# Optimization experiments

Hardware: AMD Instinct MI355X
Metric: run time of the kernel (lower is better)

## Reference

```python
import jax, jax.numpy as jnp
import numpy as np

V, L, E, H = 32000, 32, 512, 512   # vocab, nb_labels, emb_dim, hidden per direction (hidden_dim//2)
B, T = 128, 512
BOS_TAG, EOS_TAG = 1, 2


def setup_inputs() -> dict:
    key = jax.random.key(0)
    ks = jax.random.split(key, 10)
    def s(k, shape, scale=0.05):
        return jax.random.normal(k, shape, dtype=jnp.float32) * scale
    return {
        "x": jax.random.randint(ks[0], (B, T), 0, V),
        "mask": jnp.ones((B, T), jnp.int32),
        "emb": s(ks[1], (V, E), 0.1),
        "W_ih_f": s(ks[2], (4 * H, E)), "W_hh_f": s(ks[3], (4 * H, H)), "b_f": jnp.zeros((4 * H,), jnp.float32),
        "W_ih_b": s(ks[4], (4 * H, E)), "W_hh_b": s(ks[5], (4 * H, H)), "b_b": jnp.zeros((4 * H,), jnp.float32),
        "W_out": s(ks[6], (L, 2 * H)), "b_out": jnp.zeros((L,), jnp.float32),
        "transitions": s(ks[7], (L, L), 0.1),
    }


def _lstm_dir(x_emb, W_ih, W_hh, b, reverse):
    # x_emb: [B, T, E] -> hidden states [B, T, H]
    Bn = x_emb.shape[0]
    Hn = W_hh.shape[1]
    def cell(carry, x_t):
        h, c = carry
        g = x_t @ W_ih.T + h @ W_hh.T + b          # [B, 4H]
        i, f, gg, o = jnp.split(g, 4, axis=-1)
        c = jax.nn.sigmoid(f) * c + jax.nn.sigmoid(i) * jnp.tanh(gg)
        h = jax.nn.sigmoid(o) * jnp.tanh(c)
        return (h, c), h
    init = (jnp.zeros((Bn, Hn), x_emb.dtype), jnp.zeros((Bn, Hn), x_emb.dtype))
    _, hs = jax.lax.scan(cell, init, x_emb.transpose(1, 0, 2), reverse=reverse)
    return hs.transpose(1, 0, 2)


def _emissions(x, emb, W_ih_f, W_hh_f, b_f, W_ih_b, W_hh_b, b_b, W_out, b_out):
    xe = emb[x]                                    # [B, T, E]
    hf = _lstm_dir(xe, W_ih_f, W_hh_f, b_f, False)
    hb = _lstm_dir(xe, W_ih_b, W_hh_b, b_b, True)
    h = jnp.concatenate([hf, hb], axis=-1)         # [B, T, 2H]
    return h @ W_out.T + b_out                     # [B, T, L]


def _viterbi_decode(em, trans, mask):
    # em: [B, T, L]; trans[prev, next]; returns (score [B], path [B, T])
    m = mask.astype(em.dtype)
    alphas = trans[BOS_TAG][None, :] + em[:, 0]    # [B, L]
    def step(alphas, inp):
        e_t, m_t = inp                             # [B, L], [B]
        scores = alphas[:, :, None] + trans[None] + e_t[:, None, :]  # [B, Lprev, Lnext]
        new = scores.max(axis=1)
        bp = scores.argmax(axis=1).astype(jnp.int32)
        alphas = m_t[:, None] * new + (1.0 - m_t[:, None]) * alphas
        return alphas, (bp, m_t)
    alphas, (bps, ms) = jax.lax.scan(
        step, alphas, (em[:, 1:].transpose(1, 0, 2), m[:, 1:].T))
    final = alphas + trans[:, EOS_TAG][None, :]
    score = final.max(axis=-1)                     # [B]
    last_tag = final.argmax(axis=-1).astype(jnp.int32)
    def back(tag, inp):
        bp_t, m_t = inp
        prev = jnp.take_along_axis(bp_t, tag[:, None], axis=1)[:, 0]
        tag = jnp.where(m_t > 0, prev, tag)
        return tag, tag
    _, traced = jax.lax.scan(back, last_tag, (bps, ms), reverse=True)  # [T-1, B]
    path = jnp.concatenate([traced.transpose(1, 0), last_tag[:, None]], axis=1)
    return score, path


def reference(x, mask, emb, W_ih_f, W_hh_f, b_f, W_ih_b, W_hh_b, b_b, W_out, b_out, transitions):
    em = _emissions(x, emb, W_ih_f, W_hh_f, b_f, W_ih_b, W_hh_b, b_b, W_out, b_out)
    return _viterbi_decode(em, transitions, mask)
```

## Files before the change

### kernel.cpp

```cpp
#include <hip/hip_runtime.h>
#include <math.h>

namespace {
constexpr int BATCH = 128;
constexpr int SEQ   = 512;
constexpr int NL    = 32;
constexpr int BOSTAG = 1;
constexpr int EOSTAG = 2;
}

#define AL(p)    __hip_atomic_load((p),       __ATOMIC_RELAXED, __HIP_MEMORY_SCOPE_AGENT)
#define AS(p, v) __hip_atomic_store((p), (v), __ATOMIC_RELAXED, __HIP_MEMORY_SCOPE_AGENT)
#define AADD(p)  __hip_atomic_fetch_add((p), 1u, __ATOMIC_RELAXED, __HIP_MEMORY_SCOPE_AGENT)

__device__ unsigned g_sub[4][8][32];
__device__ unsigned g_root[4][32];

__global__ void reset_cnt_kernel() {
  const int i = threadIdx.x;
  ((unsigned*)g_sub)[i] = 0u;
  if (i < 4 * 32) ((unsigned*)g_root)[i] = 0u;
}

__device__ __forceinline__ void gbar(int g, int sub, unsigned epoch) {
  __syncthreads();
  if (threadIdx.x == 0) {
    const unsigned old = AADD(&g_sub[g][sub][0]);
    if (old == 8u * epoch - 1u)
      AADD(&g_root[g][0]);
    while (AL(&g_root[g][0]) < 8u * epoch)
      __builtin_amdgcn_s_sleep(2);
  }
  __builtin_amdgcn_fence(__ATOMIC_ACQUIRE, "agent");
  __syncthreads();
}

__global__ __launch_bounds__(512, 1)
void bilstm_coop(const int* __restrict__ x,
                 const float* __restrict__ emb,
                 const float* __restrict__ Wih_f, const float* __restrict__ Whh_f, const float* __restrict__ bf,
                 const float* __restrict__ Wih_b, const float* __restrict__ Whh_b, const float* __restrict__ bbias,
                 const float* __restrict__ Wout, const float* __restrict__ bout,
                 float* __restrict__ hbuf, float* __restrict__ em)
{
  __shared__ float4 WT4[8192];
  __shared__ float  em_red[512];
  float* WTf = (float*)WT4;

  const int tid = threadIdx.x, bi = blockIdx.x;
  const int rX = bi & 7, qX = bi >> 3;
  const int grp = rX >> 1;
  const int dir = grp >> 1, bh = grp & 1;
  const int ug  = (qX << 1) | (rX & 1);
  const int u0  = ug * 8, b_base = bh * 64;
  const int bb  = b_base + ug;
  const int sub = ug >> 3;

  const float* Wih = dir ? Wih_b : Wih_f;
  const float* Whh = dir ? Whh_b : Whh_f;
  const float* bv  = dir ? bbias : bf;

  for (int idx = tid; idx < 32768; idx += 512) {
    const int k = idx >> 5, r = idx & 31;
    const int gate = r & 3, uu = r >> 2;
    const int grow = gate * 512 + u0 + uu;
    const float v = (k < 512) ? Wih[(size_t)grow * 512 + k]
                              : Whh[(size_t)grow * 512 + (k - 512)];
    WTf[k * 32 + ((uu ^ ((k >> 2) & 7)) << 2) + gate] = v;
  }

  const int ks   = tid & 7;
  const int ug2  = (tid >> 3) & 3;
  const int bq   = ((tid >> 5) & 1) + 2 * (tid >> 6);
  const int bB   = b_base + 4 * bq;
  const int wb0 = 32 * ks + ((2 * ug2 + 0) ^ ks);
  const int wb1 = 32 * ks + ((2 * ug2 + 1) ^ ks);
  const int u_own = u0 + 2 * ug2 + (ks & 1);
  const int b_own = bB + (ks >> 1);
  const int l_ = tid >> 4, kc = tid & 15;

  float bias_g[4];
  #pragma unroll
  for (int g = 0; g < 4; ++g) bias_g[g] = bv[g * 512 + u_own];
  float cstate = 0.f;

  AS(&hbuf[131072 + dir * 65536 + (size_t)bb * 512 + tid], 0.f);
  unsigned epoch = 1;
  gbar(grp, sub, epoch); ++epoch;

  for (int s = 0; s < SEQ; ++s) {
    const int t = dir ? (SEQ - 1 - s) : s;

    const float* e0 = emb + (size_t)x[(bB + 0) * SEQ + t] * 512 + 4 * ks;
    const float* e1 = emb + (size_t)x[(bB + 1) * SEQ + t] * 512 + 4 * ks;
    const float* e2 = emb + (size_t)x[(bB + 2) * SEQ + t] * 512 + 4 * ks;
    const float* e3 = emb + (size_t)x[(bB + 3) * SEQ + t] * 512 + 4 * ks;
    float4 cur[4], nxt[4];
    cur[0] = *(const float4*)e0; cur[1] = *(const float4*)e1;
    cur[2] = *(const float4*)e2; cur[3] = *(const float4*)e3;

    gbar(grp, sub, epoch); ++epoch;

    const float* hprev = hbuf + (size_t)((s + 1) & 1) * 131072 + dir * 65536;
    float*       hout  = hbuf + (size_t)((s    ) & 1) * 131072 + dir * 65536;

    if (s > 0) {
      const float* hb2 = hprev + (size_t)bb * 512 + kc * 32;
      float4 hq[8];
      #pragma unroll
      for (int q = 0; q < 8; ++q) hq[q] = *(const float4*)(hb2 + q * 4);
      const float* wr_ = Wout + (size_t)l_ * 1024 + dir * 512 + kc * 32;
      float emP = 0.f;
      #pragma unroll
      for (int q = 0; q < 8; ++q) {
        const float4 wv = *(const float4*)&wr_[q * 4];
        emP = fmaf(hq[q].x, wv.x, emP);
        emP = fmaf(hq[q].y, wv.y, emP);
        emP = fmaf(hq[q].z, wv.z, emP);
        emP = fmaf(hq[q].w, wv.w, emP);
      }
      em_red[kc * 32 + l_] = emP;
    }
    __syncthreads();
    if (s > 0 && tid < 32) {
      float p = 0.f;
      #pragma unroll
      for (int ksi = 0; ksi < 16; ++ksi) p += em_red[ksi * 32 + tid];
      const int te = dir ? (SEQ - s) : (s - 1);
      if (!dir) p += bout[tid];
      atomicAdd(em + ((size_t)bb * SEQ + te) * NL + tid, p);
    }

    const float* h0 = hprev + (size_t)(bB + 0) * 512 + 4 * ks;
    const float* h1 = hprev + (size_t)(bB + 1) * 512 + 4 * ks;
    const float* h2 = hprev + (size_t)(bB + 2) * 512 + 4 * ks;
    const float* h3 = hprev + (size_t)(bB + 3) * 512 + 4 * ks;

    float acc0[4][4], acc1[4][4];
    #pragma unroll
    for (int r = 0; r < 4; ++r)
      #pragma unroll
      for (int g = 0; g < 4; ++g) { acc0[r][g] = 0.f; acc1[r][g] = 0.f; }

    #pragma unroll 2
    for (int i = 0; i < 16; ++i) {
      if (i < 15) {
        nxt[0] = *(const float4*)(e0 + (i + 1) * 32);
        nxt[1] = *(const float4*)(e1 + (i + 1) * 32);
        nxt[2] = *(const float4*)(e2 + (i + 1) * 32);
        nxt[3] = *(const float4*)(e3 + (i + 1) * 32);
      } else {
        nxt[0] = *(const float4*)h0; nxt[1] = *(const float4*)h1;
        nxt[2] = *(const float4*)h2; nxt[3] = *(const float4*)h3;
      }
      #pragma unroll
      for (int j = 0; j < 4; ++j) {
        const float4 w0 = WT4[wb0 + 256 * i + 8 * j];
        const float4 w1 = WT4[wb1 + 256 * i + 8 * j];
        #pragma unroll
        for (int r = 0; r < 4; ++r) {
          const float a = (j == 0) ? cur[r].x : (j == 1) ? cur[r].y : (j == 2) ? cur[r].z : cur[r].w;
          acc0[r][0] = fmaf(w0.x, a, acc0[r][0]);
          acc0[r][1] = fmaf(w0.y, a, acc0[r][1]);
          acc0[r][2] = fmaf(w0.z, a, acc0[r][2]);
          acc0[r][3] = fmaf(w0.w, a, acc0[r][3]);
          acc1[r][0] = fmaf(w1.x, a, acc1[r][0]);
          acc1[r][1] = fmaf(w1.y, a, acc1[r][1]);
          acc1[r][2] = fmaf(w1.z, a, acc1[r][2]);
          acc1[r][3] = fmaf(w1.w, a, acc1[r][3]);
        }
      }
      #pragma unroll
      for (int r = 0; r < 4; ++r) cur[r] = nxt[r];
    }
    #pragma unroll 2
    for (int i = 0; i < 16; ++i) {
      if (i < 15) {
        nxt[0] = *(const float4*)(h0 + (i + 1) * 32);
        nxt[1] = *(const float4*)(h1 + (i + 1) * 32);
        nxt[2] = *(const float4*)(h2 + (i + 1) * 32);
        nxt[3] = *(const float4*)(h3 + (i + 1) * 32);
      }
      #pragma unroll
      for (int j = 0; j < 4; ++j) {
        const float4 w0 = WT4[4096 + wb0 + 256 * i + 8 * j];
        const float4 w1 = WT4[4096 + wb1 + 256 * i + 8 * j];
        #pragma unroll
        for (int r = 0; r < 4; ++r) {
          const float a = (j == 0) ? cur[r].x : (j == 1) ? cur[r].y : (j == 2) ? cur[r].z : cur[r].w;
          acc0[r][0] = fmaf(w0.x, a, acc0[r][0]);
          acc0[r][1] = fmaf(w0.y, a, acc0[r][1]);
          acc0[r][2] = fmaf(w0.z, a, acc0[r][2]);
          acc0[r][3] = fmaf(w0.w, a, acc0[r][3]);
          acc1[r][0] = fmaf(w1.x, a, acc1[r][0]);
          acc1[r][1] = fmaf(w1.y, a, acc1[r][1]);
          acc1[r][2] = fmaf(w1.z, a, acc1[r][2]);
          acc1[r][3] = fmaf(w1.w, a, acc1[r][3]);
        }
      }
      #pragma unroll
      for (int r = 0; r < 4; ++r) cur[r] = nxt[r];
    }

    #pragma unroll
    for (int m = 1; m < 8; m <<= 1)
      #pragma unroll
      for (int r = 0; r < 4; ++r)
        #pragma unroll
        for (int g = 0; g < 4; ++g) {
          acc0[r][g] += __shfl_xor(acc0[r][g], m, 64);
          acc1[r][g] += __shfl_xor(acc1[r][g], m, 64);
        }

    {
      float g4[4];
      #pragma unroll
      for (int g = 0; g < 4; ++g) {
        float v = acc0[0][g];
        v = (ks == 1) ? acc1[0][g] : v;
        v = (ks == 2) ? acc0[1][g] : v;
        v = (ks == 3) ? acc1[1][g] : v;
        v = (ks == 4) ? acc0[2][g] : v;
        v = (ks == 5) ? acc1[2][g] : v;
        v = (ks == 6) ? acc0[3][g] : v;
        v = (ks == 7) ? acc1[3][g] : v;
        g4[g] = v;
      }
      const float gi = g4[0] + bias_g[0];
      const float gf = g4[1] + bias_g[1];
      const float gg = g4[2] + bias_g[2];
      const float go = g4[3] + bias_g[3];
      const float si = 1.f / (1.f + expf(-gi));
      const float sf = 1.f / (1.f + expf(-gf));
      const float so = 1.f / (1.f + expf(-go));
      cstate = sf * cstate + si * tanhf(gg);
      AS(&hout[(size_t)b_own * 512 + u_own], so * tanhf(cstate));
    }
  }
  gbar(grp, sub, epoch); ++epoch;

  {
    const float* hb2 = hbuf + 131072 + dir * 65536 + (size_t)bb * 512 + kc * 32;
    const float* wr_ = Wout + (size_t)l_ * 1024 + dir * 512 + kc * 32;
    float emP = 0.f;
    #pragma unroll
    for (int q = 0; q < 8; ++q) {
      const float4 hv = *(const float4*)(hb2 + q * 4);
      const float4 wv = *(const float4*)&wr_[q * 4];
      emP = fmaf(hv.x, wv.x, emP);
      emP = fmaf(hv.y, wv.y, emP);
      emP = fmaf(hv.z, wv.z, emP);
      emP = fmaf(hv.w, wv.w, emP);
    }
    em_red[kc * 32 + l_] = emP;
    __syncthreads();
    if (tid < 32) {
      float p = 0.f;
      #pragma unroll
      for (int ksi = 0; ksi < 16; ++ksi) p += em_red[ksi * 32 + tid];
      const int te = dir ? 0 : (SEQ - 1);
      if (!dir) p += bout[tid];
      atomicAdd(em + ((size_t)bb * SEQ + te) * NL + tid, p);
    }
  }
}

__global__ __launch_bounds__(64)
void viterbi_kernel(const float* __restrict__ em, const int* __restrict__ mask,
                    const float* __restrict__ trans, float* __restrict__ out)
{
  __shared__ float tr[32][33];
  __shared__ float alpha[32];
  __shared__ float fin[32];
  __shared__ unsigned char bp[SEQ][32];
  __shared__ float path[SEQ];

  const int b = blockIdx.x, tid = threadIdx.x;
  for (int i = tid; i < 1024; i += 64) tr[i >> 5][i & 31] = trans[i];
  __syncthreads();

  const float* emB = em + (size_t)b * SEQ * NL;
  if (tid < 32) alpha[tid] = tr[BOSTAG][tid] + emB[tid];
  __syncthreads();

  for (int t = 1; t < SEQ; ++t) {
    float best = -INFINITY, e = 0.f;
    int arg = 0;
    if (tid < 32) {
      e = emB[t * NL + tid];
      #pragma unroll 4
      for (int p = 0; p < 32; ++p) {
        const float sc = (alpha[p] + tr[p][tid]) + e;
        if (sc > best) { best = sc; arg = p; }
      }
    }
    __syncthreads();
    if (tid < 32) {
      const float m = (float)mask[b * SEQ + t];
      alpha[tid] = m * best + (1.f - m) * alpha[tid];
      bp[t][tid] = (unsigned char)arg;
    }
    __syncthreads();
  }

  if (tid < 32) fin[tid] = alpha[tid] + tr[tid][EOSTAG];
  __syncthreads();

  if (tid == 0) {
    float best = fin[0]; int tag = 0;
    for (int n = 1; n < 32; ++n) if (fin[n] > best) { best = fin[n]; tag = n; }
    out[b] = best;
    path[SEQ - 1] = (float)tag;
    for (int k = SEQ - 2; k >= 0; --k) {
      const int prev = bp[k + 1][tag];
      if (mask[b * SEQ + k + 1] > 0) tag = prev;
      path[k] = (float)tag;
    }
  }
  __syncthreads();
  for (int idx = tid; idx < SEQ; idx += 64)
    out[BATCH + (size_t)b * SEQ + idx] = path[idx];
}

extern "C" void kernel_launch(void* const* d_in, const int* in_sizes, int n_in,
                              void* d_out, int out_size, void* d_ws, size_t ws_size,
                              hipStream_t stream) {
  (void)in_sizes; (void)n_in; (void)out_size; (void)ws_size;
  const int*   x     = (const int*)d_in[0];
  const int*   mask  = (const int*)d_in[1];
  const float* emb   = (const float*)d_in[2];
  const float* Wih_f = (const float*)d_in[3];
  const float* Whh_f = (const float*)d_in[4];
  const float* bf    = (const float*)d_in[5];
  const float* Wih_b = (const float*)d_in[6];
  const float* Whh_b = (const float*)d_in[7];
  const float* bb    = (const float*)d_in[8];
  const float* Wout  = (const float*)d_in[9];
  const float* bout  = (const float*)d_in[10];
  const float* trans = (const float*)d_in[11];
  float* out  = (float*)d_out;
  float* hbuf = (float*)d_ws;
  float* em   = hbuf + 262144;

  reset_cnt_kernel<<<dim3(1), dim3(1024), 0, stream>>>();
  hipMemsetAsync(em, 0, (size_t)2097152 * sizeof(float), stream);

  void* args[] = { (void*)&x, (void*)&emb,
                   (void*)&Wih_f, (void*)&Whh_f, (void*)&bf,
                   (void*)&Wih_b, (void*)&Whh_b, (void*)&bb,
                   (void*)&Wout, (void*)&bout,
                   (void*)&hbuf, (void*)&em };
  hipLaunchCooperativeKernel((void*)bilstm_coop, dim3(256), dim3(512), args, 0, stream);
  viterbi_kernel<<<dim3(128), dim3(64), 0, stream>>>(em, mask, trans, out);
}
```

Measured before the change: 20.66 ms.

## Split LSTM work into 1024-thread blocks handling both directions with 4 units each

Each block now runs 1024 threads, the two halves serving the forward and backward direction, and owns 4 hidden units instead of 8. That halves per-thread FMA work and weight tile per direction. The grid barrier groups drop from four to two, with 16 sub-counters per group. The aim is more threads per CU to hide latency and less serial arithmetic per step, at the cost of barriers spanning twice as many blocks and a reworked weight layout in LDS.

```diff
diff --git a/kernel.cpp b/kernel.cpp
--- a/kernel.cpp
+++ b/kernel.cpp
@@ -13,13 +13,13 @@
 #define AS(p, v) __hip_atomic_store((p), (v), __ATOMIC_RELAXED, __HIP_MEMORY_SCOPE_AGENT)
 #define AADD(p)  __hip_atomic_fetch_add((p), 1u, __ATOMIC_RELAXED, __HIP_MEMORY_SCOPE_AGENT)
 
-__device__ unsigned g_sub[4][8][32];
-__device__ unsigned g_root[4][32];
+__device__ unsigned g_sub[2][16][32];
+__device__ unsigned g_root[2][32];
 
 __global__ void reset_cnt_kernel() {
   const int i = threadIdx.x;
   ((unsigned*)g_sub)[i] = 0u;
-  if (i < 4 * 32) ((unsigned*)g_root)[i] = 0u;
+  if (i < 64) ((unsigned*)g_root)[i] = 0u;
 }
 
 __device__ __forceinline__ void gbar(int g, int sub, unsigned epoch) {
@@ -28,14 +28,14 @@
     const unsigned old = AADD(&g_sub[g][sub][0]);
     if (old == 8u * epoch - 1u)
       AADD(&g_root[g][0]);
-    while (AL(&g_root[g][0]) < 8u * epoch)
+    while (AL(&g_root[g][0]) < 16u * epoch)
       __builtin_amdgcn_s_sleep(2);
   }
   __builtin_amdgcn_fence(__ATOMIC_ACQUIRE, "agent");
   __syncthreads();
 }
 
-__global__ __launch_bounds__(512, 1)
+__global__ __launch_bounds__(1024, 4)
 void bilstm_coop(const int* __restrict__ x,
                  const float* __restrict__ emb,
                  const float* __restrict__ Wih_f, const float* __restrict__ Whh_f, const float* __restrict__ bf,
@@ -43,50 +43,62 @@
                  const float* __restrict__ Wout, const float* __restrict__ bout,
                  float* __restrict__ hbuf, float* __restrict__ em)
 {
-  __shared__ float4 WT4[8192];
-  __shared__ float  em_red[512];
-  float* WTf = (float*)WT4;
+  __shared__ float4 WT4[2][4096];
+  __shared__ float  em_red[2][512];
 
   const int tid = threadIdx.x, bi = blockIdx.x;
-  const int rX = bi & 7, qX = bi >> 3;
-  const int grp = rX >> 1;
-  const int dir = grp >> 1, bh = grp & 1;
-  const int ug  = (qX << 1) | (rX & 1);
-  const int u0  = ug * 8, b_base = bh * 64;
-  const int bb  = b_base + ug;
-  const int sub = ug >> 3;
+  const int dir = tid >> 9;
+  const int tl  = tid & 511;
+  const int bh  = bi & 1;
+  const int ublock = bi >> 1;
+  const int u0  = ublock * 4, b_base = bh * 64;
+  const int p   = ublock & 1;
+  const int bb  = b_base + (ublock >> 1);
+  const int sub = ublock >> 3;
 
   const float* Wih = dir ? Wih_b : Wih_f;
   const float* Whh = dir ? Whh_b : Whh_f;
   const float* bv  = dir ? bbias : bf;
 
-  for (int idx = tid; idx < 32768; idx += 512) {
-    const int k = idx >> 5, r = idx & 31;
-    const int gate = r & 3, uu = r >> 2;
-    const int grow = gate * 512 + u0 + uu;
-    const float v = (k < 512) ? Wih[(size_t)grow * 512 + k]
-                              : Whh[(size_t)grow * 512 + (k - 512)];
-    WTf[k * 32 + ((uu ^ ((k >> 2) & 7)) << 2) + gate] = v;
-  }
-
-  const int ks   = tid & 7;
-  const int ug2  = (tid >> 3) & 3;
-  const int bq   = ((tid >> 5) & 1) + 2 * (tid >> 6);
+  {
+    float4* WTd = WT4[dir];
+    for (int n = tl; n < 4096; n += 512) {
+      const int k = n >> 2, uu = n & 3;
+      const int idx = ((k >> 3) << 5) + (((k >> 2) & 1) << 2) + ((k & 3) << 3) + uu;
+      float4 v;
+      if (k < 512) {
+        v.x = Wih[(size_t)(0 * 512 + u0 + uu) * 512 + k];
+        v.y = Wih[(size_t)(1 * 512 + u0 + uu) * 512 + k];
+        v.z = Wih[(size_t)(2 * 512 + u0 + uu) * 512 + k];
+        v.w = Wih[(size_t)(3 * 512 + u0 + uu) * 512 + k];
+      } else {
+        const int kk = k - 512;
+        v.x = Whh[(size_t)(0 * 512 + u0 + uu) * 512 + kk];
+        v.y = Whh[(size_t)(1 * 512 + u0 + uu) * 512 + kk];
+        v.z = Whh[(size_t)(2 * 512 + u0 + uu) * 512 + kk];
+        v.w = Whh[(size_t)(3 * 512 + u0 + uu) * 512 + kk];
+      }
+      WTd[idx] = v;
+    }
+  }
+  const float4* WTd = WT4[dir];
+
+  const int ks   = tl & 7;
+  const int ug2  = (tl >> 3) & 3;
+  const int bq   = tl >> 5;
   const int bB   = b_base + 4 * bq;
-  const int wb0 = 32 * ks + ((2 * ug2 + 0) ^ ks);
-  const int wb1 = 32 * ks + ((2 * ug2 + 1) ^ ks);
-  const int u_own = u0 + 2 * ug2 + (ks & 1);
-  const int b_own = bB + (ks >> 1);
-  const int l_ = tid >> 4, kc = tid & 15;
+  const int wb   = ((ks >> 1) << 5) + ((ks & 1) << 2) + ug2;
+  const int l_ = tl >> 4, kc = tl & 15;
 
   float bias_g[4];
   #pragma unroll
-  for (int g = 0; g < 4; ++g) bias_g[g] = bv[g * 512 + u_own];
+  for (int g = 0; g < 4; ++g) bias_g[g] = bv[g * 512 + u0 + ug2];
   float cstate = 0.f;
 
-  AS(&hbuf[131072 + dir * 65536 + (size_t)bb * 512 + tid], 0.f);
+  if (tl < 256)
+    AS(&hbuf[131072 + dir * 65536 + (size_t)bb * 512 + p * 256 + tl], 0.f);
   unsigned epoch = 1;
-  gbar(grp, sub, epoch); ++epoch;
+  gbar(bh, sub, epoch); ++epoch;
 
   for (int s = 0; s < SEQ; ++s) {
     const int t = dir ? (SEQ - 1 - s) : s;
@@ -99,36 +111,34 @@
     cur[0] = *(const float4*)e0; cur[1] = *(const float4*)e1;
     cur[2] = *(const float4*)e2; cur[3] = *(const float4*)e3;
 
-    gbar(grp, sub, epoch); ++epoch;
+    gbar(bh, sub, epoch); ++epoch;
 
     const float* hprev = hbuf + (size_t)((s + 1) & 1) * 131072 + dir * 65536;
     float*       hout  = hbuf + (size_t)((s    ) & 1) * 131072 + dir * 65536;
 
     if (s > 0) {
-      const float* hb2 = hprev + (size_t)bb * 512 + kc * 32;
-      float4 hq[8];
-      #pragma unroll
-      for (int q = 0; q < 8; ++q) hq[q] = *(const float4*)(hb2 + q * 4);
-      const float* wr_ = Wout + (size_t)l_ * 1024 + dir * 512 + kc * 32;
+      const float* hb2 = hprev + (size_t)bb * 512 + p * 256 + kc * 16;
+      const float* wr_ = Wout + (size_t)l_ * 1024 + dir * 512 + p * 256 + kc * 16;
       float emP = 0.f;
       #pragma unroll
-      for (int q = 0; q < 8; ++q) {
-        const float4 wv = *(const float4*)&wr_[q * 4];
-        emP = fmaf(hq[q].x, wv.x, emP);
-        emP = fmaf(hq[q].y, wv.y, emP);
-        emP = fmaf(hq[q].z, wv.z, emP);
-        emP = fmaf(hq[q].w, wv.w, emP);
-      }
-      em_red[kc * 32 + l_] = emP;
+      for (int q = 0; q < 4; ++q) {
+        const float4 hv = *(const float4*)(hb2 + q * 4);
+        const float4 wv = *(const float4*)(wr_ + q * 4);
+        emP = fmaf(hv.x, wv.x, emP);
+        emP = fmaf(hv.y, wv.y, emP);
+        emP = fmaf(hv.z, wv.z, emP);
+        emP = fmaf(hv.w, wv.w, emP);
+      }
+      em_red[dir][kc * 32 + l_] = emP;
     }
     __syncthreads();
-    if (s > 0 && tid < 32) {
-      float p = 0.f;
-      #pragma unroll
-      for (int ksi = 0; ksi < 16; ++ksi) p += em_red[ksi * 32 + tid];
+    if (s > 0 && tl < 32) {
+      float pr = 0.f;
+      #pragma unroll
+      for (int ksi = 0; ksi < 16; ++ksi) pr += em_red[dir][ksi * 32 + tl];
       const int te = dir ? (SEQ - s) : (s - 1);
-      if (!dir) p += bout[tid];
-      atomicAdd(em + ((size_t)bb * SEQ + te) * NL + tid, p);
+      if (!dir && p == 0) pr += bout[tl];
+      atomicAdd(em + ((size_t)bb * SEQ + te) * NL + tl, pr);
     }
 
     const float* h0 = hprev + (size_t)(bB + 0) * 512 + 4 * ks;
@@ -136,11 +146,11 @@
     const float* h2 = hprev + (size_t)(bB + 2) * 512 + 4 * ks;
     const float* h3 = hprev + (size_t)(bB + 3) * 512 + 4 * ks;
 
-    float acc0[4][4], acc1[4][4];
+    float acc[4][4];
     #pragma unroll
     for (int r = 0; r < 4; ++r)
       #pragma unroll
-      for (int g = 0; g < 4; ++g) { acc0[r][g] = 0.f; acc1[r][g] = 0.f; }
+      for (int g = 0; g < 4; ++g) acc[r][g] = 0.f;
 
     #pragma unroll 2
     for (int i = 0; i < 16; ++i) {
@@ -155,19 +165,15 @@
       }
       #pragma unroll
       for (int j = 0; j < 4; ++j) {
-        const float4 w0 = WT4[wb0 + 256 * i + 8 * j];
-        const float4 w1 = WT4[wb1 + 256 * i + 8 * j];
+        const float4 w0 = WTd[wb + 128 * i + 8 * j];
         #pragma unroll
         for (int r = 0; r < 4; ++r) {
-          const float a = (j == 0) ? cur[r].x : (j == 1) ? cur[r].y : (j == 2) ? cur[r].z : cur[r].w;
-          acc0[r][0] = fmaf(w0.x, a, acc0[r][0]);
-          acc0[r][1] = fmaf(w0.y, a, acc0[r][1]);
-          acc0[r][2] = fmaf(w0.z, a, acc0[r][2]);
-          acc0[r][3] = fmaf(w0.w, a, acc0[r][3]);
-          acc1[r][0] = fmaf(w1.x, a, acc1[r][0]);
-          acc1[r][1] = fmaf(w1.y, a, acc1[r][1]);
-          acc1[r][2] = fmaf(w1.z, a, acc1[r][2]);
-          acc1[r][3] = fmaf(w1.w, a, acc1[r][3]);
+          const float a = (j == 0) ? cur[r].x : (j == 1) ? cur[r].y
+                        : (j == 2) ? cur[r].z : cur[r].w;
+          acc[r][0] = fmaf(w0.x, a, acc[r][0]);
+          acc[r][1] = fmaf(w0.y, a, acc[r][1]);
+          acc[r][2] = fmaf(w0.z, a, acc[r][2]);
+          acc[r][3] = fmaf(w0.w, a, acc[r][3]);
         }
       }
       #pragma unroll
@@ -183,19 +189,15 @@
       }
       #pragma unroll
       for (int j = 0; j < 4; ++j) {
-        const float4 w0 = WT4[4096 + wb0 + 256 * i + 8 * j];
-        const float4 w1 = WT4[4096 + wb1 + 256 * i + 8 * j];
+        const float4 w0 = WTd[2048 + wb + 128 * i + 8 * j];
         #pragma unroll
         for (int r = 0; r < 4; ++r) {
-          const float a = (j == 0) ? cur[r].x : (j == 1) ? cur[r].y : (j == 2) ? cur[r].z : cur[r].w;
-          acc0[r][0] = fmaf(w0.x, a, acc0[r][0]);
-          acc0[r][1] = fmaf(w0.y, a, acc0[r][1]);
-          acc0[r][2] = fmaf(w0.z, a, acc0[r][2]);
-          acc0[r][3] = fmaf(w0.w, a, acc0[r][3]);
-          acc1[r][0] = fmaf(w1.x, a, acc1[r][0]);
-          acc1[r][1] = fmaf(w1.y, a, acc1[r][1]);
-          acc1[r][2] = fmaf(w1.z, a, acc1[r][2]);
-          acc1[r][3] = fmaf(w1.w, a, acc1[r][3]);
+          const float a = (j == 0) ? cur[r].x : (j == 1) ? cur[r].y
+                        : (j == 2) ? cur[r].z : cur[r].w;
+          acc[r][0] = fmaf(w0.x, a, acc[r][0]);
+          acc[r][1] = fmaf(w0.y, a, acc[r][1]);
+          acc[r][2] = fmaf(w0.z, a, acc[r][2]);
+          acc[r][3] = fmaf(w0.w, a, acc[r][3]);
         }
       }
       #pragma unroll
@@ -207,23 +209,17 @@
       #pragma unroll
       for (int r = 0; r < 4; ++r)
         #pragma unroll
-        for (int g = 0; g < 4; ++g) {
-          acc0[r][g] += __shfl_xor(acc0[r][g], m, 64);
-          acc1[r][g] += __shfl_xor(acc1[r][g], m, 64);
-        }
+        for (int g = 0; g < 4; ++g)
+          acc[r][g] += __shfl_xor(acc[r][g], m, 64);
 
     {
       float g4[4];
       #pragma unroll
       for (int g = 0; g < 4; ++g) {
-        float v = acc0[0][g];
-        v = (ks == 1) ? acc1[0][g] : v;
-        v = (ks == 2) ? acc0[1][g] : v;
-        v = (ks == 3) ? acc1[1][g] : v;
-        v = (ks == 4) ? acc0[2][g] : v;
-        v = (ks == 5) ? acc1[2][g] : v;
-        v = (ks == 6) ? acc0[3][g] : v;
-        v = (ks == 7) ? acc1[3][g] : v;
+        float v = acc[0][g];
+        v = (ks == 1) ? acc[1][g] : v;
+        v = (ks == 2) ? acc[2][g] : v;
+        v = (ks == 3) ? acc[3][g] : v;
         g4[g] = v;
       }
       const float gi = g4[0] + bias_g[0];
@@ -234,33 +230,34 @@
       const float sf = 1.f / (1.f + expf(-gf));
       const float so = 1.f / (1.f + expf(-go));
       cstate = sf * cstate + si * tanhf(gg);
-      AS(&hout[(size_t)b_own * 512 + u_own], so * tanhf(cstate));
-    }
-  }
-  gbar(grp, sub, epoch); ++epoch;
+      if (ks < 4)
+        AS(&hout[(size_t)(bB + ks) * 512 + u0 + ug2], so * tanhf(cstate));
+    }
+  }
+  gbar(bh, sub, epoch); ++epoch;
 
   {
-    const float* hb2 = hbuf + 131072 + dir * 65536 + (size_t)bb * 512 + kc * 32;
-    const float* wr_ = Wout + (size_t)l_ * 1024 + dir * 512 + kc * 32;
+    const float* hb2 = hbuf + 131072 + dir * 65536 + (size_t)bb * 512 + p * 256 + kc * 16;
+    const float* wr_ = Wout + (size_t)l_ * 1024 + dir * 512 + p * 256 + kc * 16;
     float emP = 0.f;
     #pragma unroll
-    for (int q = 0; q < 8; ++q) {
+    for (int q = 0; q < 4; ++q) {
       const float4 hv = *(const float4*)(hb2 + q * 4);
-      const float4 wv = *(const float4*)&wr_[q * 4];
+      const float4 wv = *(const float4*)(wr_ + q * 4);
       emP = fmaf(hv.x, wv.x, emP);
       emP = fmaf(hv.y, wv.y, emP);
       emP = fmaf(hv.z, wv.z, emP);
       emP = fmaf(hv.w, wv.w, emP);
     }
-    em_red[kc * 32 + l_] = emP;
+    em_red[dir][kc * 32 + l_] = emP;
     __syncthreads();
-    if (tid < 32) {
-      float p = 0.f;
-      #pragma unroll
-      for (int ksi = 0; ksi < 16; ++ksi) p += em_red[ksi * 32 + tid];
+    if (tl < 32) {
+      float pr = 0.f;
+      #pragma unroll
+      for (int ksi = 0; ksi < 16; ++ksi) pr += em_red[dir][ksi * 32 + tl];
       const int te = dir ? 0 : (SEQ - 1);
-      if (!dir) p += bout[tid];
-      atomicAdd(em + ((size_t)bb * SEQ + te) * NL + tid, p);
+      if (!dir && p == 0) pr += bout[tl];
+      atomicAdd(em + ((size_t)bb * SEQ + te) * NL + tl, pr);
     }
   }
 }
@@ -350,6 +347,6 @@
                    (void*)&Wih_b, (void*)&Whh_b, (void*)&bb,
                    (void*)&Wout, (void*)&bout,
                    (void*)&hbuf, (void*)&em };
-  hipLaunchCooperativeKernel((void*)bilstm_coop, dim3(256), dim3(512), args, 0, stream);
+  hipLaunchCooperativeKernel((void*)bilstm_coop, dim3(256), dim3(1024), args, 0, stream);
   viterbi_kernel<<<dim3(128), dim3(64), 0, stream>>>(em, mask, trans, out);
 }
```

New measurement: 29.52 ms. 42.9% more time.
